# Performance work log

Measured on AMD Instinct MI355X. Metric: run time of the kernel, lower is better.

## Reference

```python
import jax, jax.numpy as jnp
import numpy as np

N_NODES = 100000
N_EDGES = 1600000
F = 128


def setup_inputs() -> dict:
    key = jax.random.key(0)
    ks = jax.random.split(key, 8)
    edge_src = jax.random.randint(ks[0], (N_EDGES,), 0, N_NODES, dtype=jnp.int32)
    edge_dst = jax.random.randint(ks[1], (N_EDGES,), 0, N_NODES, dtype=jnp.int32)
    edge_vals = jax.random.uniform(ks[2], (N_EDGES,), dtype=jnp.float32)
    feats = jax.random.normal(ks[3], (N_NODES, F), dtype=jnp.float32)
    s = 1.0 / np.sqrt(F)
    W1 = jax.random.normal(ks[4], (F, F), dtype=jnp.float32) * s
    b1 = jax.random.normal(ks[5], (F,), dtype=jnp.float32) * s
    W2 = jax.random.normal(ks[6], (F, F), dtype=jnp.float32) * s
    b2 = jax.random.normal(ks[7], (F,), dtype=jnp.float32) * s
    return {"edge_src": edge_src, "edge_dst": edge_dst, "edge_vals": edge_vals,
            "feats": feats, "W1": W1, "b1": b1, "W2": W2, "b2": b2}


def reference(edge_src, edge_dst, edge_vals, feats, W1, b1, W2, b2):
    # LE = L @ feats  (SpMM over COO edges: dst <- sum val * feats[src])
    msgs = edge_vals[:, None] * jnp.take(feats, edge_src, axis=0)  # [E, F]
    LE = jax.ops.segment_sum(msgs, edge_dst, num_segments=feats.shape[0])  # [N, F]
    # sf_E = (L + I) @ feats = LE + feats  (SelfLoop is identity)
    sf_E = LE + feats
    left_part = sf_E @ W1.T + b1          # W1(sf_E)
    E = LE * feats                        # torch.mul(LE, feats)
    right_part = E @ W2.T + b2            # W2(E)
    return left_part + right_part
```

## Files before the change

### kernel.cpp

```cpp
#include <hip/hip_runtime.h>

#define N_NODES 100000
#define N_EDGES 1600000
#define F 128
#define M_PAD 100032
#define NCB 391
#define CAP 8192
#define EPB 4096
#define FB_BLOCKS 25000
#define W_BLOCKS 64

typedef __attribute__((ext_vector_type(8))) short short8;
typedef __attribute__((ext_vector_type(4))) float float4v;

__device__ __forceinline__ unsigned pack_bf16(float x, float y) {
    unsigned ux = __float_as_uint(x), uy = __float_as_uint(y);
    ux = (ux + 0x7fffu + ((ux >> 16) & 1u)) >> 16;
    uy = (uy + 0x7fffu + ((uy >> 16) & 1u)) >> 16;
    return ux | (uy << 16);
}

__global__ __launch_bounds__(256) void prep_kernel(
    const float2* __restrict__ feats2, unsigned* __restrict__ featsb,
    const float* __restrict__ W1, const float* __restrict__ W2,
    unsigned* __restrict__ Wbu, int* __restrict__ ccur)
{
    int b = blockIdx.x, t = threadIdx.x;
    if (b < FB_BLOCKS) {
        int i = b * 256 + t;
        float2 v = feats2[i];
        featsb[i] = pack_bf16(v.x, v.y);
    } else if (b < FB_BLOCKS + W_BLOCKS) {
        int i = (b - FB_BLOCKS) * 256 + t;
        int j = i >> 7, c = i & 127;
        const float* s = (c < 64) ? &W1[j * 128 + 2 * c] : &W2[j * 128 + 2 * (c - 64)];
        Wbu[i] = pack_bf16(s[0], s[1]);
    } else {
        int i = (b - FB_BLOCKS - W_BLOCKS) * 256 + t;
        if (i < NCB) ccur[i] = i * CAP;
    }
}

__global__ __launch_bounds__(256) void passA_kernel(
    const int* __restrict__ esrc, const int* __restrict__ edst,
    const float* __restrict__ evals, int* __restrict__ ccur,
    int2* __restrict__ srtA)
{
    __shared__ int2 sv[EPB];
    __shared__ unsigned short bkt[EPB];
    __shared__ int h[NCB], lo[NCB], gbase[NCB];

    const int t = threadIdx.x;
    const int base = blockIdx.x * EPB;
    const int cnt = min(EPB, N_EDGES - base);

    for (int i = t; i < NCB; i += 256) h[i] = 0;
    __syncthreads();

    int rsrc[16], rdst[16], rrank[16];
    float rval[16];
#pragma unroll
    for (int i = 0; i < 16; i++) {
        int e = base + i * 256 + t;
        if (e < N_EDGES) {
            rsrc[i] = esrc[e];
            rdst[i] = edst[e];
            rval[i] = evals[e];
            rrank[i] = atomicAdd(&h[rdst[i] >> 8], 1);
        } else rdst[i] = -1;
    }
    __syncthreads();

    if (t < 64) {
        int carry = 0;
        for (int b0 = 0; b0 < NCB; b0 += 64) {
            int i = b0 + t;
            int x = (i < NCB) ? h[i] : 0;
            int v = x;
#pragma unroll
            for (int d = 1; d < 64; d <<= 1) {
                int y = __shfl_up(v, d);
                if (t >= d) v += y;
            }
            if (i < NCB) lo[i] = v - x + carry;
            carry += __shfl(v, 63);
        }
    }
    __syncthreads();

#pragma unroll
    for (int i = 0; i < 16; i++) {
        if (rdst[i] >= 0) {
            int b = rdst[i] >> 8;
            int s = lo[b] + rrank[i];
            sv[s]  = make_int2(rsrc[i] | ((rdst[i] & 255) << 24),
                               __float_as_int(rval[i]));
            bkt[s] = (unsigned short)b;
        }
    }
    for (int b = t; b < NCB; b += 256) {
        int c = h[b];
        if (c) gbase[b] = atomicAdd(&ccur[b], c);
    }
    __syncthreads();

    for (int s = t; s < cnt; s += 256) {
        int b = bkt[s];
        srtA[gbase[b] + (s - lo[b])] = sv[s];
    }
}

__global__ __launch_bounds__(1024) void passB_kernel(
    const int* __restrict__ ccur, const int2* __restrict__ srtA,
    int2* __restrict__ srt, int2* __restrict__ bege)
{
    __shared__ int hist[256], excl[256], cur[256];
    const int t = threadIdx.x;
    const int b = blockIdx.x;
    const int base = b * CAP;
    const int cnt = ccur[b] - base;

    if (t < 256) hist[t] = 0;
    __syncthreads();
    for (int idx = t; idx < cnt; idx += 1024)
        atomicAdd(&hist[(unsigned)srtA[base + idx].x >> 24], 1);
    __syncthreads();
    if (t < 64) {
        int carry = 0;
#pragma unroll
        for (int c = 0; c < 4; c++) {
            int i = c * 64 + t;
            int x = hist[i];
            int v = x;
#pragma unroll
            for (int d = 1; d < 64; d <<= 1) {
                int y = __shfl_up(v, d);
                if (t >= d) v += y;
            }
            excl[i] = v - x + carry;
            carry += __shfl(v, 63);
        }
    }
    __syncthreads();
    if (t < 256) {
        int n = (b << 8) + t;
        if (n < N_NODES) {
            int bg = base + excl[t];
            bege[n] = make_int2(bg, bg + hist[t]);
            cur[t] = bg;
        }
    }
    __syncthreads();
    for (int idx = t; idx < cnt; idx += 1024) {
        int2 e = srtA[base + idx];
        int d = (unsigned)e.x >> 24;
        int pos = atomicAdd(&cur[d], 1);
        srt[pos] = make_int2(e.x & 0x00FFFFFF, e.y);
    }
}

__global__ __launch_bounds__(256) void gather_kernel(
    const int2* __restrict__ bege, const int2* __restrict__ srt,
    const uint2* __restrict__ fb2,
    uint2* __restrict__ Abig2)
{
    const int gw = (blockIdx.x * 256 + threadIdx.x) >> 6;
    const int lane = threadIdx.x & 63;
    const int node = gw * 2 + (lane >> 5);
    const int l = lane & 31;
    if (node >= N_NODES) return;

    int2 be = bege[node];
    int i = be.x;
    const int end = be.y;

    float a0 = 0.f, a1 = 0.f, a2 = 0.f, a3 = 0.f;
    for (; i + 3 < end; i += 4) {
        int2 e0 = srt[i], e1 = srt[i + 1], e2 = srt[i + 2], e3 = srt[i + 3];
        uint2 p0 = fb2[(size_t)e0.x * 32 + l];
        uint2 p1 = fb2[(size_t)e1.x * 32 + l];
        uint2 p2 = fb2[(size_t)e2.x * 32 + l];
        uint2 p3 = fb2[(size_t)e3.x * 32 + l];
        float v0 = __int_as_float(e0.y), v1 = __int_as_float(e1.y);
        float v2 = __int_as_float(e2.y), v3 = __int_as_float(e3.y);
        a0 += v0 * __uint_as_float(p0.x << 16) + v1 * __uint_as_float(p1.x << 16)
            + v2 * __uint_as_float(p2.x << 16) + v3 * __uint_as_float(p3.x << 16);
        a1 += v0 * __uint_as_float(p0.x & 0xffff0000u) + v1 * __uint_as_float(p1.x & 0xffff0000u)
            + v2 * __uint_as_float(p2.x & 0xffff0000u) + v3 * __uint_as_float(p3.x & 0xffff0000u);
        a2 += v0 * __uint_as_float(p0.y << 16) + v1 * __uint_as_float(p1.y << 16)
            + v2 * __uint_as_float(p2.y << 16) + v3 * __uint_as_float(p3.y << 16);
        a3 += v0 * __uint_as_float(p0.y & 0xffff0000u) + v1 * __uint_as_float(p1.y & 0xffff0000u)
            + v2 * __uint_as_float(p2.y & 0xffff0000u) + v3 * __uint_as_float(p3.y & 0xffff0000u);
    }
    for (; i < end; i++) {
        int2 e0 = srt[i];
        uint2 p0 = fb2[(size_t)e0.x * 32 + l];
        float v0 = __int_as_float(e0.y);
        a0 += v0 * __uint_as_float(p0.x << 16);
        a1 += v0 * __uint_as_float(p0.x & 0xffff0000u);
        a2 += v0 * __uint_as_float(p0.y << 16);
        a3 += v0 * __uint_as_float(p0.y & 0xffff0000u);
    }

    uint2 pf = fb2[(size_t)node * 32 + l];
    float f0 = __uint_as_float(pf.x << 16);
    float f1 = __uint_as_float(pf.x & 0xffff0000u);
    float f2v = __uint_as_float(pf.y << 16);
    float f3 = __uint_as_float(pf.y & 0xffff0000u);

    uint2 S, P;
    S.x = pack_bf16(a0 + f0, a1 + f1);  S.y = pack_bf16(a2 + f2v, a3 + f3);
    P.x = pack_bf16(a0 * f0, a1 * f1);  P.y = pack_bf16(a2 * f2v, a3 * f3);
    Abig2[(size_t)node * 64 + l]      = S;
    Abig2[(size_t)node * 64 + 32 + l] = P;
}

__global__ __launch_bounds__(256) void gemm_kernel(
    const unsigned short* __restrict__ Abig, const unsigned short* __restrict__ Wb,
    const float* __restrict__ b1, const float* __restrict__ b2,
    float* __restrict__ out)
{
    const int t = threadIdx.x;
    const int w = t >> 6, lane = t & 63;
    const int col = lane & 15;
    const int quad = lane >> 4;
    const int ko = quad * 8;
    const int m0 = blockIdx.x * 64 + w * 16;

    float4v acc[8];
#pragma unroll
    for (int j = 0; j < 8; j++) acc[j] = (float4v)(0.f);

    const unsigned short* arow = Abig + (size_t)(m0 + col) * 256 + ko;
#pragma unroll
    for (int k0 = 0; k0 < 8; k0++) {
        short8 a = *(const short8*)(arow + k0 * 32);
#pragma unroll
        for (int j = 0; j < 8; j++) {
            short8 b = *(const short8*)&Wb[(size_t)(j * 16 + col) * 256 + k0 * 32 + ko];
            acc[j] = __builtin_amdgcn_mfma_f32_16x16x32_bf16(a, b, acc[j], 0, 0, 0);
        }
    }

#pragma unroll
    for (int j = 0; j < 8; j++) {
        int n0 = j * 16 + col;
        float bb = b1[n0] + b2[n0];
#pragma unroll
        for (int r = 0; r < 4; r++) {
            int m = m0 + quad * 4 + r;
            if (m < N_NODES)
                __builtin_nontemporal_store(acc[j][r] + bb, &out[(size_t)m * F + n0]);
        }
    }
}

extern "C" void kernel_launch(void* const* d_in, const int* in_sizes, int n_in,
                              void* d_out, int out_size, void* d_ws, size_t ws_size,
                              hipStream_t stream) {
    const int*   edge_src  = (const int*)d_in[0];
    const int*   edge_dst  = (const int*)d_in[1];
    const float* edge_vals = (const float*)d_in[2];
    const float* feats     = (const float*)d_in[3];
    const float* W1        = (const float*)d_in[4];
    const float* b1        = (const float*)d_in[5];
    const float* W2        = (const float*)d_in[6];
    const float* b2        = (const float*)d_in[7];
    float* out = (float*)d_out;

    char* ws = (char*)d_ws;
    unsigned*       featsb = (unsigned*)      (ws);
    int2*           srtA   = (int2*)          (ws + 25600000);
    int2*           srt    = (int2*)          (ws + 51224576);
    int2*           bege   = (int2*)          (ws + 76849152);
    int*            ccur   = (int*)           (ws + 77649152);
    unsigned*       Wbu    = (unsigned*)      (ws + 77651200);
    unsigned short* Abig   = (unsigned short*)(ws + 77716736);

    prep_kernel<<<FB_BLOCKS + W_BLOCKS + 2, 256, 0, stream>>>(
        (const float2*)feats, featsb, W1, W2, Wbu, ccur);

    passA_kernel<<<(N_EDGES + EPB - 1) / EPB, 256, 0, stream>>>(
        edge_src, edge_dst, edge_vals, ccur, srtA);

    passB_kernel<<<NCB, 1024, 0, stream>>>(ccur, srtA, srt, bege);

    gather_kernel<<<(N_NODES / 2 * 64 + 255) / 256, 256, 0, stream>>>(
        bege, srt, (const uint2*)featsb, (uint2*)Abig);

    gemm_kernel<<<M_PAD / 64, 256, 0, stream>>>(
        Abig, (const unsigned short*)Wbu, b1, b2, out);
}
```

Before: 285.1 us.

## Fuse second sort pass into gather using LDS edge lists per 64-node bucket

Shrinks the coarse destination buckets from 256 to 64 nodes, which gives 1563 buckets of 2048 capacity. The second counting-sort pass now runs inside the gather kernel and places each bucket's edges into a shared-memory list, so the globally sorted edge array and per-node begin/end array are no longer written and re-read. Each 256-thread block then accumulates its 64 nodes straight from LDS. This removes one kernel launch and a full pass of global traffic over the edges, at the cost of 16KB of LDS per block and fewer nodes processed in parallel per block. The diff also changes prep_kernel's launch to 7 CC_BLOCKS and relies on its hidden body initialising 1563 ccur entries, which cannot be checked here.

```diff
diff --git a/kernel.cpp b/kernel.cpp
--- a/kernel.cpp
+++ b/kernel.cpp
@@ -4,11 +4,12 @@
 #define N_EDGES 1600000
 #define F 128
 #define M_PAD 100032
-#define NCB 391
-#define CAP 8192
+#define NCB 1563
+#define CAP 2048
 #define EPB 4096
 #define FB_BLOCKS 25000
 #define W_BLOCKS 64
+#define CC_BLOCKS 7
 
 typedef __attribute__((ext_vector_type(8))) short short8;
 typedef __attribute__((ext_vector_type(4))) float float4v;
@@ -66,7 +67,7 @@
             rsrc[i] = esrc[e];
             rdst[i] = edst[e];
             rval[i] = evals[e];
-            rrank[i] = atomicAdd(&h[rdst[i] >> 8], 1);
+            rrank[i] = atomicAdd(&h[rdst[i] >> 6], 1);
         } else rdst[i] = -1;
     }
     __syncthreads();
@@ -91,9 +92,9 @@
 #pragma unroll
     for (int i = 0; i < 16; i++) {
         if (rdst[i] >= 0) {
-            int b = rdst[i] >> 8;
+            int b = rdst[i] >> 6;
             int s = lo[b] + rrank[i];
-            sv[s]  = make_int2(rsrc[i] | ((rdst[i] & 255) << 24),
+            sv[s]  = make_int2(rsrc[i] | ((rdst[i] & 63) << 24),
                                __float_as_int(rval[i]));
             bkt[s] = (unsigned short)b;
         }
@@ -110,109 +111,99 @@
     }
 }
 
-__global__ __launch_bounds__(1024) void passB_kernel(
+__global__ __launch_bounds__(256) void fused_gather_kernel(
     const int* __restrict__ ccur, const int2* __restrict__ srtA,
-    int2* __restrict__ srt, int2* __restrict__ bege)
-{
-    __shared__ int hist[256], excl[256], cur[256];
+    const uint2* __restrict__ fb2,
+    uint2* __restrict__ Abig2)
+{
+    __shared__ int2 list[CAP];
+    __shared__ int hist[64], cur[64];
+
     const int t = threadIdx.x;
     const int b = blockIdx.x;
     const int base = b * CAP;
     const int cnt = ccur[b] - base;
 
-    if (t < 256) hist[t] = 0;
-    __syncthreads();
-    for (int idx = t; idx < cnt; idx += 1024)
-        atomicAdd(&hist[(unsigned)srtA[base + idx].x >> 24], 1);
-    __syncthreads();
+    if (t < 64) hist[t] = 0;
+    __syncthreads();
+
+    for (int i = t; i < cnt; i += 256)
+        atomicAdd(&hist[(unsigned)srtA[base + i].x >> 24], 1);
+    __syncthreads();
+
     if (t < 64) {
-        int carry = 0;
-#pragma unroll
-        for (int c = 0; c < 4; c++) {
-            int i = c * 64 + t;
-            int x = hist[i];
-            int v = x;
-#pragma unroll
-            for (int d = 1; d < 64; d <<= 1) {
-                int y = __shfl_up(v, d);
-                if (t >= d) v += y;
-            }
-            excl[i] = v - x + carry;
-            carry += __shfl(v, 63);
-        }
-    }
-    __syncthreads();
-    if (t < 256) {
-        int n = (b << 8) + t;
-        if (n < N_NODES) {
-            int bg = base + excl[t];
-            bege[n] = make_int2(bg, bg + hist[t]);
-            cur[t] = bg;
-        }
-    }
-    __syncthreads();
-    for (int idx = t; idx < cnt; idx += 1024) {
-        int2 e = srtA[base + idx];
+        int x = hist[t], v = x;
+#pragma unroll
+        for (int d = 1; d < 64; d <<= 1) {
+            int y = __shfl_up(v, d);
+            if (t >= d) v += y;
+        }
+        cur[t] = v - x;
+    }
+    __syncthreads();
+
+    for (int i = t; i < cnt; i += 256) {
+        int2 e = srtA[base + i];
         int d = (unsigned)e.x >> 24;
         int pos = atomicAdd(&cur[d], 1);
-        srt[pos] = make_int2(e.x & 0x00FFFFFF, e.y);
-    }
-}
-
-__global__ __launch_bounds__(256) void gather_kernel(
-    const int2* __restrict__ bege, const int2* __restrict__ srt,
-    const uint2* __restrict__ fb2,
-    uint2* __restrict__ Abig2)
-{
-    const int gw = (blockIdx.x * 256 + threadIdx.x) >> 6;
-    const int lane = threadIdx.x & 63;
-    const int node = gw * 2 + (lane >> 5);
+        list[pos] = make_int2(e.x & 0x00FFFFFF, e.y);
+    }
+    __syncthreads();
+
+    const int w = t >> 6;
+    const int lane = t & 63;
+    const int h = lane >> 5;
     const int l = lane & 31;
-    if (node >= N_NODES) return;
-
-    int2 be = bege[node];
-    int i = be.x;
-    const int end = be.y;
-
-    float a0 = 0.f, a1 = 0.f, a2 = 0.f, a3 = 0.f;
-    for (; i + 3 < end; i += 4) {
-        int2 e0 = srt[i], e1 = srt[i + 1], e2 = srt[i + 2], e3 = srt[i + 3];
-        uint2 p0 = fb2[(size_t)e0.x * 32 + l];
-        uint2 p1 = fb2[(size_t)e1.x * 32 + l];
-        uint2 p2 = fb2[(size_t)e2.x * 32 + l];
-        uint2 p3 = fb2[(size_t)e3.x * 32 + l];
-        float v0 = __int_as_float(e0.y), v1 = __int_as_float(e1.y);
-        float v2 = __int_as_float(e2.y), v3 = __int_as_float(e3.y);
-        a0 += v0 * __uint_as_float(p0.x << 16) + v1 * __uint_as_float(p1.x << 16)
-            + v2 * __uint_as_float(p2.x << 16) + v3 * __uint_as_float(p3.x << 16);
-        a1 += v0 * __uint_as_float(p0.x & 0xffff0000u) + v1 * __uint_as_float(p1.x & 0xffff0000u)
-            + v2 * __uint_as_float(p2.x & 0xffff0000u) + v3 * __uint_as_float(p3.x & 0xffff0000u);
-        a2 += v0 * __uint_as_float(p0.y << 16) + v1 * __uint_as_float(p1.y << 16)
-            + v2 * __uint_as_float(p2.y << 16) + v3 * __uint_as_float(p3.y << 16);
-        a3 += v0 * __uint_as_float(p0.y & 0xffff0000u) + v1 * __uint_as_float(p1.y & 0xffff0000u)
-            + v2 * __uint_as_float(p2.y & 0xffff0000u) + v3 * __uint_as_float(p3.y & 0xffff0000u);
-    }
-    for (; i < end; i++) {
-        int2 e0 = srt[i];
-        uint2 p0 = fb2[(size_t)e0.x * 32 + l];
-        float v0 = __int_as_float(e0.y);
-        a0 += v0 * __uint_as_float(p0.x << 16);
-        a1 += v0 * __uint_as_float(p0.x & 0xffff0000u);
-        a2 += v0 * __uint_as_float(p0.y << 16);
-        a3 += v0 * __uint_as_float(p0.y & 0xffff0000u);
-    }
-
-    uint2 pf = fb2[(size_t)node * 32 + l];
-    float f0 = __uint_as_float(pf.x << 16);
-    float f1 = __uint_as_float(pf.x & 0xffff0000u);
-    float f2v = __uint_as_float(pf.y << 16);
-    float f3 = __uint_as_float(pf.y & 0xffff0000u);
-
-    uint2 S, P;
-    S.x = pack_bf16(a0 + f0, a1 + f1);  S.y = pack_bf16(a2 + f2v, a3 + f3);
-    P.x = pack_bf16(a0 * f0, a1 * f1);  P.y = pack_bf16(a2 * f2v, a3 * f3);
-    Abig2[(size_t)node * 64 + l]      = S;
-    Abig2[(size_t)node * 64 + 32 + l] = P;
+
+#pragma unroll
+    for (int np = 0; np < 16; np += 2) {
+        const int nl = w * 16 + np + h;
+        const int end = cur[nl];
+        int i = end - hist[nl];
+
+        float a0 = 0.f, a1 = 0.f, a2 = 0.f, a3 = 0.f;
+        for (; i + 3 < end; i += 4) {
+            int2 e0 = list[i], e1 = list[i + 1], e2 = list[i + 2], e3 = list[i + 3];
+            uint2 p0 = fb2[(size_t)e0.x * 32 + l];
+            uint2 p1 = fb2[(size_t)e1.x * 32 + l];
+            uint2 p2 = fb2[(size_t)e2.x * 32 + l];
+            uint2 p3 = fb2[(size_t)e3.x * 32 + l];
+            float v0 = __int_as_float(e0.y), v1 = __int_as_float(e1.y);
+            float v2 = __int_as_float(e2.y), v3 = __int_as_float(e3.y);
+            a0 += v0 * __uint_as_float(p0.x << 16) + v1 * __uint_as_float(p1.x << 16)
+                + v2 * __uint_as_float(p2.x << 16) + v3 * __uint_as_float(p3.x << 16);
+            a1 += v0 * __uint_as_float(p0.x & 0xffff0000u) + v1 * __uint_as_float(p1.x & 0xffff0000u)
+                + v2 * __uint_as_float(p2.x & 0xffff0000u) + v3 * __uint_as_float(p3.x & 0xffff0000u);
+            a2 += v0 * __uint_as_float(p0.y << 16) + v1 * __uint_as_float(p1.y << 16)
+                + v2 * __uint_as_float(p2.y << 16) + v3 * __uint_as_float(p3.y << 16);
+            a3 += v0 * __uint_as_float(p0.y & 0xffff0000u) + v1 * __uint_as_float(p1.y & 0xffff0000u)
+                + v2 * __uint_as_float(p2.y & 0xffff0000u) + v3 * __uint_as_float(p3.y & 0xffff0000u);
+        }
+        for (; i < end; i++) {
+            int2 e0 = list[i];
+            uint2 p0 = fb2[(size_t)e0.x * 32 + l];
+            float v0 = __int_as_float(e0.y);
+            a0 += v0 * __uint_as_float(p0.x << 16);
+            a1 += v0 * __uint_as_float(p0.x & 0xffff0000u);
+            a2 += v0 * __uint_as_float(p0.y << 16);
+            a3 += v0 * __uint_as_float(p0.y & 0xffff0000u);
+        }
+
+        const int gn = b * 64 + nl;
+        if (gn < N_NODES) {
+            uint2 pf = fb2[(size_t)gn * 32 + l];
+            float f0 = __uint_as_float(pf.x << 16);
+            float f1 = __uint_as_float(pf.x & 0xffff0000u);
+            float f2v = __uint_as_float(pf.y << 16);
+            float f3 = __uint_as_float(pf.y & 0xffff0000u);
+
+            uint2 S, P;
+            S.x = pack_bf16(a0 + f0, a1 + f1);  S.y = pack_bf16(a2 + f2v, a3 + f3);
+            P.x = pack_bf16(a0 * f0, a1 * f1);  P.y = pack_bf16(a2 * f2v, a3 * f3);
+            Abig2[(size_t)gn * 64 + l]      = S;
+            Abig2[(size_t)gn * 64 + 32 + l] = P;
+        }
+    }
 }
 
 __global__ __launch_bounds__(256) void gemm_kernel(
@@ -271,22 +262,18 @@
     char* ws = (char*)d_ws;
     unsigned*       featsb = (unsigned*)      (ws);
     int2*           srtA   = (int2*)          (ws + 25600000);
-    int2*           srt    = (int2*)          (ws + 51224576);
-    int2*           bege   = (int2*)          (ws + 76849152);
-    int*            ccur   = (int*)           (ws + 77649152);
-    unsigned*       Wbu    = (unsigned*)      (ws + 77651200);
-    unsigned short* Abig   = (unsigned short*)(ws + 77716736);
-
-    prep_kernel<<<FB_BLOCKS + W_BLOCKS + 2, 256, 0, stream>>>(
+    int*            ccur   = (int*)           (ws + 51208192);
+    unsigned*       Wbu    = (unsigned*)      (ws + 51216384);
+    unsigned short* Abig   = (unsigned short*)(ws + 51281920);
+
+    prep_kernel<<<FB_BLOCKS + W_BLOCKS + CC_BLOCKS, 256, 0, stream>>>(
         (const float2*)feats, featsb, W1, W2, Wbu, ccur);
 
     passA_kernel<<<(N_EDGES + EPB - 1) / EPB, 256, 0, stream>>>(
         edge_src, edge_dst, edge_vals, ccur, srtA);
 
-    passB_kernel<<<NCB, 1024, 0, stream>>>(ccur, srtA, srt, bege);
-
-    gather_kernel<<<(N_NODES / 2 * 64 + 255) / 256, 256, 0, stream>>>(
-        bege, srt, (const uint2*)featsb, (uint2*)Abig);
+    fused_gather_kernel<<<NCB, 256, 0, stream>>>(
+        ccur, srtA, (const uint2*)featsb, (uint2*)Abig);
 
     gemm_kernel<<<M_PAD / 64, 256, 0, stream>>>(
         Abig, (const unsigned short*)Wbu, b1, b2, out);
```

Result: faster. 279.4 us (-2.0%).
